# Performance work log

Measured on AMD Instinct MI355X. Metric: run time of the kernel, lower is better.

## Reference

```python
import jax, jax.numpy as jnp
import numpy as np
from jax import lax

VOL, PATCH, DIM, DEPTH, HEADS, DIM_HEAD, MLP, CH, B = 64, 8, 768, 4, 12, 64, 3072, 1, 2
INNER = HEADS * DIM_HEAD
GS = VOL // PATCH              # 8 -> N = 512 tokens
EPS = 1e-5


def _sincos_1d(embed_dim, pos):
    omega = np.arange(embed_dim // 2, dtype=float) / (embed_dim / 2.0)
    omega = 1.0 / 10000 ** omega
    out = np.einsum('m,d->md', pos.reshape(-1), omega)
    return np.concatenate([np.sin(out), np.cos(out)], axis=1)


def _pos_embed_3d(embed_dim, gs):
    gd = np.arange(gs, dtype=np.float32)
    gh = np.arange(gs, dtype=np.float32)
    gw = np.arange(gs, dtype=np.float32)
    grid = np.stack(np.meshgrid(gw, gh, gd), axis=0).reshape([3, 1, gs, gs, gs])
    emb = np.concatenate([_sincos_1d(embed_dim // 3, grid[i]) for i in range(3)], axis=1)
    return jnp.asarray(emb, jnp.float32)[None]  # [1, N, dim]


def setup_inputs() -> dict:
    key = jax.random.key(0)
    ks = jax.random.split(key, 12)
    s = 0.02  # xavier-like small init scale
    d = {
        'volume': jax.random.normal(ks[0], (B, CH, VOL, VOL, VOL), jnp.float32),
        'conv_w': jax.random.normal(ks[1], (DIM, CH, PATCH, PATCH, PATCH), jnp.float32) * s,
        'conv_b': jnp.zeros((DIM,), jnp.float32),
        'pos_embed': _pos_embed_3d(DIM, GS),
        'ln1_w': jnp.ones((DEPTH, DIM), jnp.float32),
        'ln1_b': jnp.zeros((DEPTH, DIM), jnp.float32),
        'w_qkv': jax.random.normal(ks[2], (DEPTH, DIM, 3 * INNER), jnp.float32) * s,
        'w_o': jax.random.normal(ks[3], (DEPTH, INNER, DIM), jnp.float32) * s,
        'b_o': jnp.zeros((DEPTH, DIM), jnp.float32),
        'ln2_w': jnp.ones((DEPTH, DIM), jnp.float32),
        'ln2_b': jnp.zeros((DEPTH, DIM), jnp.float32),
        'w1': jax.random.normal(ks[4], (DEPTH, DIM, MLP), jnp.float32) * s,
        'b1': jnp.zeros((DEPTH, MLP), jnp.float32),
        'w2': jax.random.normal(ks[5], (DEPTH, MLP, DIM), jnp.float32) * s,
        'b2': jnp.zeros((DEPTH, DIM), jnp.float32),
        'lnf_w': jnp.ones((DIM,), jnp.float32),
        'lnf_b': jnp.zeros((DIM,), jnp.float32),
    }
    return d


def _ln(x, w, b):
    m = jnp.mean(x, axis=-1, keepdims=True)
    v = jnp.mean(jnp.square(x - m), axis=-1, keepdims=True)
    return (x - m) * lax.rsqrt(v + EPS) * w + b


def _forward(volume, conv_w, conv_b, pos_embed, ln1_w, ln1_b, w_qkv, w_o, b_o,
             ln2_w, ln2_b, w1, b1, w2, b2, lnf_w, lnf_b):
    # Conv3d patch embedding (stride == kernel == patch)
    x = lax.conv_general_dilated(volume, conv_w, window_strides=(PATCH,) * 3,
                                 padding='VALID',
                                 dimension_numbers=('NCDHW', 'OIDHW', 'NCDHW'))
    x = x + conv_b[None, :, None, None, None]
    b = x.shape[0]
    x = x.reshape(b, DIM, -1).transpose(0, 2, 1)   # b (d h w) c -> [B, N, dim]
    x = x + pos_embed
    scale = DIM_HEAD ** -0.5

    def layer(x, p):
        l1w, l1b, wqkv, wo, bo, l2w, l2b, W1, B1, W2, B2 = p
        h = _ln(x, l1w, l1b)
        qkv = h @ wqkv                               # [B, N, 3*inner]
        q, k, v = jnp.split(qkv, 3, axis=-1)
        def heads(t):
            bsz, n, _ = t.shape
            return t.reshape(bsz, n, HEADS, DIM_HEAD).transpose(0, 2, 1, 3)
        q, k, v = heads(q), heads(k), heads(v)
        attn = jax.nn.softmax(jnp.einsum('bhqd,bhkd->bhqk', q, k) * scale, axis=-1)
        o = jnp.einsum('bhqk,bhkd->bhqd', attn, v)   # [B, H, N, dh]
        o = o.transpose(0, 2, 1, 3).reshape(x.shape[0], -1, INNER)
        x = x + (o @ wo + bo)
        h = _ln(x, l2w, l2b)
        x = x + (jnp.tanh(h @ W1 + B1) @ W2 + B2)
        return x, None

    params = (ln1_w, ln1_b, w_qkv, w_o, b_o, ln2_w, ln2_b, w1, b1, w2, b2)
    x, _ = lax.scan(layer, x, params)
    return _ln(x, lnf_w, lnf_b)


def reference(volume, conv_w, conv_b, pos_embed, ln1_w, ln1_b, w_qkv, w_o, b_o,
              ln2_w, ln2_b, w1, b1, w2, b2, lnf_w, lnf_b):
    return _forward(volume, conv_w, conv_b, pos_embed, ln1_w, ln1_b, w_qkv, w_o, b_o,
                    ln2_w, ln2_b, w1, b1, w2, b2, lnf_w, lnf_b)
```

## Files before the change

### kernel.cpp

```cpp
#include <hip/hip_runtime.h>
#include <hip/hip_bf16.h>

typedef __hip_bfloat16 bf16;
typedef short bf16x8 __attribute__((ext_vector_type(8)));
typedef float f32x4 __attribute__((ext_vector_type(4)));

__device__ __forceinline__ float b2f(bf16 v) { return __bfloat162float(v); }
__device__ __forceinline__ void storev(float* p, float v) { *p = v; }
__device__ __forceinline__ void storev(bf16* p, float v) { *p = __float2bfloat16(v); }

__device__ __forceinline__ void store4(float* p, float a, float b, float c, float d) {
  *(float4*)p = make_float4(a, b, c, d);
}
__device__ __forceinline__ void store4(bf16* p, float a, float b, float c, float d) {
  bf16 pk[4] = {__float2bfloat16(a), __float2bfloat16(b), __float2bfloat16(c),
                __float2bfloat16(d)};
  *(uint2*)p = *(uint2*)pk;
}

__device__ __forceinline__ void gl2lds16(const bf16* g, bf16* l) {
  __builtin_amdgcn_global_load_lds(
      (const __attribute__((address_space(1))) unsigned int*)g,
      (__attribute__((address_space(3))) unsigned int*)l, 16, 0, 0);
}
__device__ __forceinline__ void gl2lds16f(const float* g, float* l) {
  __builtin_amdgcn_global_load_lds(
      (const __attribute__((address_space(1))) unsigned int*)g,
      (__attribute__((address_space(3))) unsigned int*)l, 16, 0, 0);
}

__global__ __launch_bounds__(256) void prologue_all(
    const float* __restrict__ wqkv, const float* __restrict__ wo,
    const float* __restrict__ w1, const float* __restrict__ w2,
    bf16* __restrict__ tqkv, bf16* __restrict__ two,
    bf16* __restrict__ t1, bf16* __restrict__ t2,
    const float* __restrict__ convw, bf16* __restrict__ cwb,
    const float* __restrict__ vol, bf16* __restrict__ patchA) {
  int bid = blockIdx.x;
  size_t L = blockIdx.y;
  int tid = threadIdx.x;

  if (bid >= 864) {
    if (bid < 960) {
      int cid = (bid - 864) * 4 + (int)L;
      int i = (cid * 256 + tid) * 4;
      float4 v = *(const float4*)&convw[i];
      bf16 pk[4] = {__float2bfloat16(v.x), __float2bfloat16(v.y),
                    __float2bfloat16(v.z), __float2bfloat16(v.w)};
      *(uint2*)&cwb[i] = *(uint2*)pk;
    } else {
      int t = (bid - 960) * 4 + (int)L;
      int b = t >> 9, n = t & 511;
      int pd = n >> 6, ph = (n >> 3) & 7, pw = n & 7;
      const float* vb = vol + ((size_t)b << 18);
      for (int l = tid; l < 512; l += 256) {
        int i = l >> 6, j = (l >> 3) & 7, k = l & 7;
        patchA[(size_t)t * 512 + l] =
            __float2bfloat16(vb[(pd * 8 + i) * 4096 + (ph * 8 + j) * 64 + (pw * 8 + k)]);
      }
    }
    return;
  }

  const float* in;
  bf16* out;
  int R, C, tc, t0;
  if (bid < 216)       { in = wqkv + L * 768 * 2304; out = tqkv + L * 768 * 2304; R = 768;  C = 2304; tc = 36; t0 = bid; }
  else if (bid < 288)  { in = wo + L * 768 * 768;    out = two + L * 768 * 768;   R = 768;  C = 768;  tc = 12; t0 = bid - 216; }
  else if (bid < 576)  { in = w1 + L * 768 * 3072;   out = t1 + L * 768 * 3072;   R = 768;  C = 3072; tc = 48; t0 = bid - 288; }
  else                 { in = w2 + L * 3072 * 768;   out = t2 + L * 3072 * 768;   R = 3072; C = 768;  tc = 12; t0 = bid - 576; }
  int r0 = (t0 / tc) * 128, c0 = (t0 % tc) * 64;
  __shared__ float tile[8192];
#pragma unroll
  for (int it = 0; it < 8; ++it) {
    int s = tid + it * 256;
    int r = s >> 4, cc = s & 15;
    int csrc = (cc ^ ((r >> 3) & 7)) << 2;
    gl2lds16f(&in[(size_t)(r0 + r) * C + c0 + csrc], &tile[s * 4]);
  }
  __syncthreads();
#pragma unroll
  for (int it = 0; it < 4; ++it) {
    int idx = tid + it * 256;
    int c = idx >> 4, rb = (idx & 15) * 8;
    int slot = (c >> 2) ^ ((rb >> 3) & 7);
    int base = rb * 64 + slot * 4 + (c & 3);
    bf16 pk[8];
#pragma unroll
    for (int e = 0; e < 8; ++e) pk[e] = __float2bfloat16(tile[base + e * 64]);
    *(uint4*)&out[(size_t)(c0 + c) * R + r0 + rb] = *(uint4*)pk;
  }
}

template <typename OutT>
__global__ __launch_bounds__(256) void ln_kernel(const float* __restrict__ x,
                                                 const float* __restrict__ w,
                                                 const float* __restrict__ b,
                                                 OutT* __restrict__ out) {
  int row = (blockIdx.x << 2) + (threadIdx.x >> 6);
  int lane = threadIdx.x & 63;
  const float* xr = x + (size_t)row * 768;
  float4 v[3];
  float s = 0.f, ss = 0.f;
#pragma unroll
  for (int j = 0; j < 3; ++j) {
    v[j] = *(const float4*)&xr[j * 256 + lane * 4];
    s += v[j].x + v[j].y + v[j].z + v[j].w;
    ss += v[j].x * v[j].x + v[j].y * v[j].y + v[j].z * v[j].z + v[j].w * v[j].w;
  }
#pragma unroll
  for (int off = 32; off; off >>= 1) {
    s += __shfl_xor(s, off);
    ss += __shfl_xor(ss, off);
  }
  float m = s * (1.f / 768.f);
  float r = rsqrtf(ss * (1.f / 768.f) - m * m + 1e-5f);
  OutT* orow = out + (size_t)row * 768;
#pragma unroll
  for (int j = 0; j < 3; ++j) {
    int cidx = j * 256 + lane * 4;
    float4 wv = *(const float4*)&w[cidx];
    float4 bv = *(const float4*)&b[cidx];
    store4(orow + cidx,
           (v[j].x - m) * r * wv.x + bv.x,
           (v[j].y - m) * r * wv.y + bv.y,
           (v[j].z - m) * r * wv.z + bv.z,
           (v[j].w - m) * r * wv.w + bv.w);
  }
}

template <int BM, int BN, int WR, int WC, int EPI>
__global__ __launch_bounds__(256) void mfma_gemm(
    const bf16* __restrict__ A, const bf16* __restrict__ Bt,
    const float* __restrict__ bias, const float* __restrict__ aux,
    bf16* __restrict__ vt,
    void* __restrict__ Cout, int M, int N, int K) {
  constexpr int WTM = BM / WR, WTN = BN / WC;
  constexpr int MT = WTM / 16, NT = WTN / 16;
  __shared__ bf16 As[BM * 64];
  __shared__ bf16 Bs[BN * 64];
  int tid = threadIdx.x;
  int wave = tid >> 6, lane = tid & 63;
  int wm = wave / WC, wn = wave % WC;
  int m15 = lane & 15, q = lane >> 4;
  int m0 = blockIdx.y * BM, n0 = blockIdx.x * BN;
  int kspan = K / gridDim.z;
  int kbeg = blockIdx.z * kspan, kend = kbeg + kspan;

  f32x4 acc[MT][NT];
#pragma unroll
  for (int i = 0; i < MT; ++i)
#pragma unroll
    for (int j = 0; j < NT; ++j) acc[i][j] = (f32x4){0.f, 0.f, 0.f, 0.f};

  for (int k0 = kbeg; k0 < kend; k0 += 64) {
#pragma unroll
    for (int it = 0; it < BM * 8 / 256; ++it) {
      int c = tid + it * 256;
      int row = c >> 3, cc = c & 7;
      gl2lds16(&A[(size_t)(m0 + row) * K + k0 + cc * 8], &As[c * 8]);
    }
#pragma unroll
    for (int it = 0; it < BN * 8 / 256; ++it) {
      int c = tid + it * 256;
      int row = c >> 3, cc = c & 7;
      gl2lds16(&Bt[(size_t)(n0 + row) * K + k0 + cc * 8], &Bs[c * 8]);
    }
    __syncthreads();
#pragma unroll
    for (int s = 0; s < 2; ++s) {
      bf16x8 af[MT], bfr[NT];
#pragma unroll
      for (int i = 0; i < MT; ++i)
        af[i] = *(const bf16x8*)&As[(wm * WTM + i * 16 + m15) * 64 + s * 32 + q * 8];
#pragma unroll
      for (int j = 0; j < NT; ++j)
        bfr[j] = *(const bf16x8*)&Bs[(wn * WTN + j * 16 + m15) * 64 + s * 32 + q * 8];
#pragma unroll
      for (int i = 0; i < MT; ++i)
#pragma unroll
        for (int j = 0; j < NT; ++j)
          acc[i][j] = __builtin_amdgcn_mfma_f32_16x16x32_bf16(af[i], bfr[j], acc[i][j], 0, 0, 0);
    }
    __syncthreads();
  }

#pragma unroll
  for (int i = 0; i < MT; ++i) {
#pragma unroll
    for (int j = 0; j < NT; ++j) {
      int col = n0 + wn * WTN + j * 16 + m15;
      if (EPI == 4) {
        if (col < 1536) {
#pragma unroll
          for (int r = 0; r < 4; ++r) {
            int row = m0 + wm * WTM + i * 16 + q * 4 + r;
            ((bf16*)Cout)[(size_t)row * 1536 + col] = __float2bfloat16(acc[i][j][r]);
          }
        } else {
          int row0 = m0 + wm * WTM + i * 16 + q * 4;
          int cl = col - 1536;
          int hh = cl >> 6, dd = cl & 63;
          int bb = row0 >> 9, tok = row0 & 511;
          bf16 pk[4];
#pragma unroll
          for (int r = 0; r < 4; ++r) pk[r] = __float2bfloat16(acc[i][j][r]);
          *(uint2*)&vt[((size_t)(bb * 12 + hh) * 64 + dd) * 512 + tok] = *(uint2*)pk;
        }
      } else if (EPI == 5) {
        float bv = (blockIdx.z == 0) ? bias[col] : 0.f;
#pragma unroll
        for (int r = 0; r < 4; ++r) {
          int row = m0 + wm * WTM + i * 16 + q * 4 + r;
          unsafeAtomicAdd(&((float*)Cout)[(size_t)row * N + col], acc[i][j][r] + bv);
        }
      } else {
        float bv = (EPI == 0) ? 0.f : bias[col];
#pragma unroll
        for (int r = 0; r < 4; ++r) {
          int row = m0 + wm * WTM + i * 16 + q * 4 + r;
          float v = acc[i][j][r] + bv;
          if (EPI == 2) v = tanhf(v);
          if (EPI == 3) v += aux[(size_t)(row & 511) * N + col];
          if (EPI == 0 || EPI == 2)
            ((bf16*)Cout)[(size_t)row * N + col] = __float2bfloat16(v);
          else
            ((float*)Cout)[(size_t)row * N + col] = v;
        }
      }
    }
  }
}

__global__ __launch_bounds__(128) void attn_mfma(const bf16* __restrict__ qk,
                                                 const bf16* __restrict__ Vt,
                                                 bf16* __restrict__ o) {
  constexpr int PS = 520;
  __shared__ bf16 KVs[64 * 64];
  __shared__ bf16 P[32 * PS];
  int bh = blockIdx.x;
  int b = bh / 12, hh = bh % 12;
  int q0 = blockIdx.y * 32;
  int tid = threadIdx.x;
  int wave = tid >> 6, lane = tid & 63;
  int n15 = lane & 15, quad = lane >> 4;
  const bf16* qkb = qk + (size_t)b * 512 * 1536;
  int ql = wave * 16 + n15;

  const bf16* qp = qkb + (size_t)(q0 + ql) * 1536 + hh * 64 + quad * 8;
  bf16x8 qf0 = *(const bf16x8*)qp;
  bf16x8 qf1 = *(const bf16x8*)(qp + 32);

  f32x4 S[32];
#pragma unroll
  for (int i = 0; i < 32; ++i) S[i] = (f32x4){0.f, 0.f, 0.f, 0.f};

  const bf16* kbase = qkb + 768 + hh * 64;
#pragma unroll
  for (int kc = 0; kc < 8; ++kc) {
    __syncthreads();
#pragma unroll
    for (int it = 0; it < 4; ++it) {
      int c = tid + it * 128;
      int r = c >> 3, cc = c & 7;
      gl2lds16(&kbase[(size_t)(kc * 64 + r) * 1536 + cc * 8], &KVs[c * 8]);
    }
    __syncthreads();
#pragma unroll
    for (int t = 0; t < 4; ++t) {
      int idx = kc * 4 + t;
      bf16x8 a0 = *(const bf16x8*)&KVs[(t * 16 + n15) * 64 + quad * 8];
      bf16x8 a1 = *(const bf16x8*)&KVs[(t * 16 + n15) * 64 + 32 + quad * 8];
      S[idx] = __builtin_amdgcn_mfma_f32_16x16x32_bf16(a0, qf0, S[idx], 0, 0, 0);
      S[idx] = __builtin_amdgcn_mfma_f32_16x16x32_bf16(a1, qf1, S[idx], 0, 0, 0);
    }
  }

  float mx = -1e30f;
#pragma unroll
  for (int i = 0; i < 32; ++i)
#pragma unroll
    for (int r = 0; r < 4; ++r) { S[i][r] *= 0.125f; mx = fmaxf(mx, S[i][r]); }
  mx = fmaxf(mx, __shfl_xor(mx, 16));
  mx = fmaxf(mx, __shfl_xor(mx, 32));
  float sum = 0.f;
#pragma unroll
  for (int i = 0; i < 32; ++i)
#pragma unroll
    for (int r = 0; r < 4; ++r) { float e = __expf(S[i][r] - mx); S[i][r] = e; sum += e; }
  sum += __shfl_xor(sum, 16);
  sum += __shfl_xor(sum, 32);
  float inv = 1.f / sum;

#pragma unroll
  for (int i = 0; i < 32; ++i) {
    bf16 pk[4];
#pragma unroll
    for (int r = 0; r < 4; ++r) pk[r] = __float2bfloat16(S[i][r] * inv);
    *(uint2*)&P[(size_t)ql * PS + i * 16 + quad * 4] = *(uint2*)pk;
  }

  f32x4 oacc[4];
#pragma unroll
  for (int dt = 0; dt < 4; ++dt) oacc[dt] = (f32x4){0.f, 0.f, 0.f, 0.f};
  const bf16* vtb = Vt + (size_t)bh * 64 * 512;
  for (int kc = 0; kc < 8; ++kc) {
    __syncthreads();
#pragma unroll
    for (int it = 0; it < 4; ++it) {
      int c = tid + it * 128;
      int r = c >> 3, cc = c & 7;
      gl2lds16(&vtb[(size_t)r * 512 + kc * 64 + cc * 8], &KVs[c * 8]);
    }
    __syncthreads();
    bf16x8 p0 = *(const bf16x8*)&P[(size_t)ql * PS + kc * 64 + quad * 8];
    bf16x8 p1 = *(const bf16x8*)&P[(size_t)ql * PS + kc * 64 + 32 + quad * 8];
#pragma unroll
    for (int dt = 0; dt < 4; ++dt) {
      bf16x8 v0 = *(const bf16x8*)&KVs[(dt * 16 + n15) * 64 + quad * 8];
      bf16x8 v1 = *(const bf16x8*)&KVs[(dt * 16 + n15) * 64 + 32 + quad * 8];
      oacc[dt] = __builtin_amdgcn_mfma_f32_16x16x32_bf16(p0, v0, oacc[dt], 0, 0, 0);
      oacc[dt] = __builtin_amdgcn_mfma_f32_16x16x32_bf16(p1, v1, oacc[dt], 0, 0, 0);
    }
  }

#pragma unroll
  for (int dt = 0; dt < 4; ++dt)
#pragma unroll
    for (int r = 0; r < 4; ++r) {
      int tok = q0 + wave * 16 + quad * 4 + r;
      o[((size_t)b * 512 + tok) * 768 + hh * 64 + dt * 16 + n15] =
          __float2bfloat16(oacc[dt][r]);
    }
}

extern "C" void kernel_launch(void* const* d_in, const int* in_sizes, int n_in,
                              void* d_out, int out_size, void* d_ws, size_t ws_size,
                              hipStream_t stream) {
  const float* volume = (const float*)d_in[0];
  const float* conv_w = (const float*)d_in[1];
  const float* conv_b = (const float*)d_in[2];
  const float* pos    = (const float*)d_in[3];
  const float* ln1w   = (const float*)d_in[4];
  const float* ln1b   = (const float*)d_in[5];
  const float* wqkv   = (const float*)d_in[6];
  const float* wo     = (const float*)d_in[7];
  const float* bo     = (const float*)d_in[8];
  const float* ln2w   = (const float*)d_in[9];
  const float* ln2b   = (const float*)d_in[10];
  const float* w1     = (const float*)d_in[11];
  const float* b1     = (const float*)d_in[12];
  const float* w2     = (const float*)d_in[13];
  const float* b2     = (const float*)d_in[14];
  const float* lnfw   = (const float*)d_in[15];
  const float* lnfb   = (const float*)d_in[16];

  char* w = (char*)d_ws;
  float* x    = (float*)(w + 0);
  bf16* h     = (bf16*)(w + 3145728);
  bf16* qk    = (bf16*)(w + 4718592);
  bf16* patchA= qk;
  bf16* Vt    = (bf16*)(w + 7864320);
  bf16* oact  = (bf16*)(w + 9437184);
  bf16* cwb   = (bf16*)(w + 15728640);
  bf16* tqkv  = (bf16*)(w + 16515072);
  bf16* two   = (bf16*)(w + 30670848);
  bf16* t1    = (bf16*)(w + 35389440);
  bf16* t2    = (bf16*)(w + 54263808);

  prologue_all<<<dim3(1216, 4), 256, 0, stream>>>(
      wqkv, wo, w1, w2, tqkv, two, t1, t2, conv_w, cwb, volume, patchA);
  mfma_gemm<64, 64, 2, 2, 3><<<dim3(12, 16), 256, 0, stream>>>(
      patchA, cwb, conv_b, pos, nullptr, x, 1024, 768, 512);

  for (int L = 0; L < 4; ++L) {
    ln_kernel<bf16><<<256, 256, 0, stream>>>(x, ln1w + L * 768, ln1b + L * 768, h);
    mfma_gemm<64, 64, 2, 2, 4><<<dim3(36, 16), 256, 0, stream>>>(
        h, tqkv + (size_t)L * 768 * 2304, nullptr, nullptr, Vt, qk, 1024, 2304, 768);
    attn_mfma<<<dim3(24, 16), 128, 0, stream>>>(qk, Vt, oact);
    mfma_gemm<64, 64, 2, 2, 5><<<dim3(12, 16, 2), 256, 0, stream>>>(
        oact, two + (size_t)L * 768 * 768, bo + L * 768, nullptr, nullptr, x, 1024, 768, 768);
    ln_kernel<bf16><<<256, 256, 0, stream>>>(x, ln2w + L * 768, ln2b + L * 768, h);
    mfma_gemm<64, 64, 2, 2, 2><<<dim3(48, 16), 256, 0, stream>>>(
        h, t1 + (size_t)L * 768 * 3072, b1 + L * 3072, nullptr, nullptr, oact, 1024, 3072, 768);
    mfma_gemm<64, 64, 2, 2, 5><<<dim3(12, 16, 4), 256, 0, stream>>>(
        oact, t2 + (size_t)L * 768 * 3072, b2 + L * 768, nullptr, nullptr, x, 1024, 768, 3072);
  }

  ln_kernel<float><<<256, 256, 0, stream>>>(x, lnfw, lnfb, (float*)d_out);
}
```

Baseline: 499.0 us.

## Defer per-layer weight transposes into earlier GEMM launches as extra blocks

The prologue now transposes and casts only layer 0's weights. Layers 1-3 are converted by extra blocks appended to the grids of the patch-embed, layer-0 QKV and layer-0 MLP1 GEMMs, so that conversion work overlaps with compute. GEMM shared memory becomes a unified buffer sized for the transpose tile when that role is active. The risk is that the larger shared allocation lowers occupancy of the host GEMMs, and that the mixed block roles leave the grid load unbalanced.

```diff
diff --git a/kernel.cpp b/kernel.cpp
--- a/kernel.cpp
+++ b/kernel.cpp
@@ -29,48 +29,23 @@
       (__attribute__((address_space(3))) unsigned int*)l, 16, 0, 0);
 }
 
-__global__ __launch_bounds__(256) void prologue_all(
-    const float* __restrict__ wqkv, const float* __restrict__ wo,
-    const float* __restrict__ w1, const float* __restrict__ w2,
-    bf16* __restrict__ tqkv, bf16* __restrict__ two,
-    bf16* __restrict__ t1, bf16* __restrict__ t2,
-    const float* __restrict__ convw, bf16* __restrict__ cwb,
-    const float* __restrict__ vol, bf16* __restrict__ patchA) {
-  int bid = blockIdx.x;
-  size_t L = blockIdx.y;
-  int tid = threadIdx.x;
-
-  if (bid >= 864) {
-    if (bid < 960) {
-      int cid = (bid - 864) * 4 + (int)L;
-      int i = (cid * 256 + tid) * 4;
-      float4 v = *(const float4*)&convw[i];
-      bf16 pk[4] = {__float2bfloat16(v.x), __float2bfloat16(v.y),
-                    __float2bfloat16(v.z), __float2bfloat16(v.w)};
-      *(uint2*)&cwb[i] = *(uint2*)pk;
-    } else {
-      int t = (bid - 960) * 4 + (int)L;
-      int b = t >> 9, n = t & 511;
-      int pd = n >> 6, ph = (n >> 3) & 7, pw = n & 7;
-      const float* vb = vol + ((size_t)b << 18);
-      for (int l = tid; l < 512; l += 256) {
-        int i = l >> 6, j = (l >> 3) & 7, k = l & 7;
-        patchA[(size_t)t * 512 + l] =
-            __float2bfloat16(vb[(pd * 8 + i) * 4096 + (ph * 8 + j) * 64 + (pw * 8 + k)]);
-      }
-    }
-    return;
-  }
-
+struct TPW {
+  const float *wqkv, *wo, *w1, *w2;
+  bf16 *tqkv, *two, *t1, *t2;
+};
+
+__device__ __forceinline__ void tp_tile_body(const TPW& p, int L, int t0all,
+                                             void* smemv, int tid) {
   const float* in;
   bf16* out;
   int R, C, tc, t0;
-  if (bid < 216)       { in = wqkv + L * 768 * 2304; out = tqkv + L * 768 * 2304; R = 768;  C = 2304; tc = 36; t0 = bid; }
-  else if (bid < 288)  { in = wo + L * 768 * 768;    out = two + L * 768 * 768;   R = 768;  C = 768;  tc = 12; t0 = bid - 216; }
-  else if (bid < 576)  { in = w1 + L * 768 * 3072;   out = t1 + L * 768 * 3072;   R = 768;  C = 3072; tc = 48; t0 = bid - 288; }
-  else                 { in = w2 + L * 3072 * 768;   out = t2 + L * 3072 * 768;   R = 3072; C = 768;  tc = 12; t0 = bid - 576; }
+  size_t Ls = (size_t)L;
+  if (t0all < 216)      { in = p.wqkv + Ls * 768 * 2304; out = p.tqkv + Ls * 768 * 2304; R = 768;  C = 2304; tc = 36; t0 = t0all; }
+  else if (t0all < 288) { in = p.wo + Ls * 768 * 768;    out = p.two + Ls * 768 * 768;   R = 768;  C = 768;  tc = 12; t0 = t0all - 216; }
+  else if (t0all < 576) { in = p.w1 + Ls * 768 * 3072;   out = p.t1 + Ls * 768 * 3072;   R = 768;  C = 3072; tc = 48; t0 = t0all - 288; }
+  else                  { in = p.w2 + Ls * 3072 * 768;   out = p.t2 + Ls * 3072 * 768;   R = 3072; C = 768;  tc = 12; t0 = t0all - 576; }
   int r0 = (t0 / tc) * 128, c0 = (t0 % tc) * 64;
-  __shared__ float tile[8192];
+  float* tile = (float*)smemv;
 #pragma unroll
   for (int it = 0; it < 8; ++it) {
     int s = tid + it * 256;
@@ -89,6 +64,35 @@
 #pragma unroll
     for (int e = 0; e < 8; ++e) pk[e] = __float2bfloat16(tile[base + e * 64]);
     *(uint4*)&out[(size_t)(c0 + c) * R + r0 + rb] = *(uint4*)pk;
+  }
+}
+
+__global__ __launch_bounds__(256) void prologue_all(
+    TPW tpw, const float* __restrict__ convw, bf16* __restrict__ cwb,
+    const float* __restrict__ vol, bf16* __restrict__ patchA) {
+  __shared__ __align__(16) float tile[8192];
+  int bid = blockIdx.x, tid = threadIdx.x;
+  if (bid < 864) {
+    tp_tile_body(tpw, 0, bid, tile, tid);
+    return;
+  }
+  if (bid < 1248) {
+    int cid = bid - 864;
+    int i = (cid * 256 + tid) * 4;
+    float4 v = *(const float4*)&convw[i];
+    bf16 pk[4] = {__float2bfloat16(v.x), __float2bfloat16(v.y),
+                  __float2bfloat16(v.z), __float2bfloat16(v.w)};
+    *(uint2*)&cwb[i] = *(uint2*)pk;
+    return;
+  }
+  int t = bid - 1248;
+  int b = t >> 9, n = t & 511;
+  int pd = n >> 6, ph = (n >> 3) & 7, pw = n & 7;
+  const float* vb = vol + ((size_t)b << 18);
+  for (int l = tid; l < 512; l += 256) {
+    int i = l >> 6, j = (l >> 3) & 7, k = l & 7;
+    patchA[(size_t)t * 512 + l] =
+        __float2bfloat16(vb[(pd * 8 + i) * 4096 + (ph * 8 + j) * 64 + (pw * 8 + k)]);
   }
 }
 
@@ -129,16 +133,26 @@
   }
 }
 
-template <int BM, int BN, int WR, int WC, int EPI>
+template <int BM, int BN, int WR, int WC, int EPI, int GX, int TPL>
 __global__ __launch_bounds__(256) void mfma_gemm(
     const bf16* __restrict__ A, const bf16* __restrict__ Bt,
     const float* __restrict__ bias, const float* __restrict__ aux,
     bf16* __restrict__ vt,
-    void* __restrict__ Cout, int M, int N, int K) {
+    void* __restrict__ Cout, int M, int N, int K, TPW tpw) {
+  constexpr bool TP = (TPL >= 0);
+  constexpr int SMEM = TP ? 32768 : (BM * 64 + BN * 64) * 2;
+  __shared__ __align__(16) char smem[SMEM];
+  if constexpr (TP) {
+    if ((int)blockIdx.x >= GX) {
+      tp_tile_body(tpw, TPL, ((int)blockIdx.x - GX) * 16 + (int)blockIdx.y,
+                   smem, threadIdx.x);
+      return;
+    }
+  }
+  bf16* As = (bf16*)smem;
+  bf16* Bs = (bf16*)(smem + (size_t)BM * 64 * 2);
   constexpr int WTM = BM / WR, WTN = BN / WC;
   constexpr int MT = WTM / 16, NT = WTN / 16;
-  __shared__ bf16 As[BM * 64];
-  __shared__ bf16 Bs[BN * 64];
   int tid = threadIdx.x;
   int wave = tid >> 6, lane = tid & 63;
   int wm = wave / WC, wn = wave % WC;
@@ -368,23 +382,32 @@
   bf16* t1    = (bf16*)(w + 35389440);
   bf16* t2    = (bf16*)(w + 54263808);
 
-  prologue_all<<<dim3(1216, 4), 256, 0, stream>>>(
-      wqkv, wo, w1, w2, tqkv, two, t1, t2, conv_w, cwb, volume, patchA);
-  mfma_gemm<64, 64, 2, 2, 3><<<dim3(12, 16), 256, 0, stream>>>(
-      patchA, cwb, conv_b, pos, nullptr, x, 1024, 768, 512);
+  TPW tpw{wqkv, wo, w1, w2, tqkv, two, t1, t2};
+
+  prologue_all<<<2272, 256, 0, stream>>>(tpw, conv_w, cwb, volume, patchA);
+  mfma_gemm<64, 64, 2, 2, 3, 12, 1><<<dim3(66, 16), 256, 0, stream>>>(
+      patchA, cwb, conv_b, pos, nullptr, x, 1024, 768, 512, tpw);
 
   for (int L = 0; L < 4; ++L) {
     ln_kernel<bf16><<<256, 256, 0, stream>>>(x, ln1w + L * 768, ln1b + L * 768, h);
-    mfma_gemm<64, 64, 2, 2, 4><<<dim3(36, 16), 256, 0, stream>>>(
-        h, tqkv + (size_t)L * 768 * 2304, nullptr, nullptr, Vt, qk, 1024, 2304, 768);
+    if (L == 0)
+      mfma_gemm<64, 64, 2, 2, 4, 36, 2><<<dim3(90, 16), 256, 0, stream>>>(
+          h, tqkv + (size_t)L * 768 * 2304, nullptr, nullptr, Vt, qk, 1024, 2304, 768, tpw);
+    else
+      mfma_gemm<64, 64, 2, 2, 4, 0, -1><<<dim3(36, 16), 256, 0, stream>>>(
+          h, tqkv + (size_t)L * 768 * 2304, nullptr, nullptr, Vt, qk, 1024, 2304, 768, tpw);
     attn_mfma<<<dim3(24, 16), 128, 0, stream>>>(qk, Vt, oact);
-    mfma_gemm<64, 64, 2, 2, 5><<<dim3(12, 16, 2), 256, 0, stream>>>(
-        oact, two + (size_t)L * 768 * 768, bo + L * 768, nullptr, nullptr, x, 1024, 768, 768);
+    mfma_gemm<64, 64, 2, 2, 5, 0, -1><<<dim3(12, 16, 2), 256, 0, stream>>>(
+        oact, two + (size_t)L * 768 * 768, bo + L * 768, nullptr, nullptr, x, 1024, 768, 768, tpw);
     ln_kernel<bf16><<<256, 256, 0, stream>>>(x, ln2w + L * 768, ln2b + L * 768, h);
-    mfma_gemm<64, 64, 2, 2, 2><<<dim3(48, 16), 256, 0, stream>>>(
-        h, t1 + (size_t)L * 768 * 3072, b1 + L * 3072, nullptr, nullptr, oact, 1024, 3072, 768);
-    mfma_gemm<64, 64, 2, 2, 5><<<dim3(12, 16, 4), 256, 0, stream>>>(
-        oact, t2 + (size_t)L * 768 * 3072, b2 + L * 768, nullptr, nullptr, x, 1024, 768, 3072);
+    if (L == 0)
+      mfma_gemm<64, 64, 2, 2, 2, 48, 3><<<dim3(102, 16), 256, 0, stream>>>(
+          h, t1 + (size_t)L * 768 * 3072, b1 + L * 3072, nullptr, nullptr, oact, 1024, 3072, 768, tpw);
+    else
+      mfma_gemm<64, 64, 2, 2, 2, 0, -1><<<dim3(48, 16), 256, 0, stream>>>(
+          h, t1 + (size_t)L * 768 * 3072, b1 + L * 3072, nullptr, nullptr, oact, 1024, 3072, 768, tpw);
+    mfma_gemm<64, 64, 2, 2, 5, 0, -1><<<dim3(12, 16, 4), 256, 0, stream>>>(
+        oact, t2 + (size_t)L * 768 * 3072, b2 + L * 768, nullptr, nullptr, x, 1024, 768, 3072, tpw);
   }
 
   ln_kernel<float><<<256, 256, 0, stream>>>(x, lnfw, lnfb, (float*)d_out);
```

Result: no change. 505.2 us (+1.2%).
